# Kernel optimization log

Hardware: AMD Instinct MI355X
Metric: run time of the kernel (lower is better)

Reference implementation:

```python
import jax, jax.numpy as jnp
import numpy as np

B, C_IN, H, W = 4, 256, 256, 256
L = 5000                 # candidate lines per image
N_PTS0, N_PTS1 = 32, 8   # sampled points per line, pooled points
DIM_LOI, DIM_FC = 128, 1024
N_OUT_LINE = 2500


def setup_inputs() -> dict:
    key = jax.random.key(0)
    ks = jax.random.split(key, 8)
    feature = jax.random.normal(ks[0], (B, C_IN, H, W), jnp.float32)
    # line endpoints in [0, 255) pixel coords (row, col)
    lines_in = jax.random.uniform(ks[1], (B, L, 2, 2), jnp.float32) * 255.0
    fc1_w = jax.random.normal(ks[2], (DIM_LOI, C_IN), jnp.float32) * 0.05
    fc1_b = jnp.zeros((DIM_LOI,), jnp.float32)
    w1 = jax.random.normal(ks[3], (DIM_FC, DIM_LOI * N_PTS1), jnp.float32) * 0.02
    b1 = jnp.zeros((DIM_FC,), jnp.float32)
    w2 = jax.random.normal(ks[4], (DIM_FC, DIM_FC), jnp.float32) * 0.02
    b2 = jnp.zeros((DIM_FC,), jnp.float32)
    w3 = jax.random.normal(ks[5], (4, DIM_FC), jnp.float32) * 0.02
    b3 = jnp.zeros((4,), jnp.float32)
    return dict(feature=feature, lines_in=lines_in, fc1_w=fc1_w, fc1_b=fc1_b,
                w1=w1, b1=b1, w2=w2, b2=b2, w3=w3, b3=b3)


def _bilinear_sample(xi, px, py):
    # xi: [C, H, W]; px, py: [P] float coords. Matches torch clamp(0, 255).
    px0 = jnp.clip(jnp.floor(px), 0.0, 255.0)
    py0 = jnp.clip(jnp.floor(py), 0.0, 255.0)
    px1 = jnp.clip(px0 + 1.0, 0.0, 255.0)
    py1 = jnp.clip(py0 + 1.0, 0.0, 255.0)
    px0l, py0l = px0.astype(jnp.int32), py0.astype(jnp.int32)
    px1l, py1l = px1.astype(jnp.int32), py1.astype(jnp.int32)
    xp = (xi[:, px0l, py0l] * (px1 - px) * (py1 - py)
          + xi[:, px1l, py0l] * (px - px0) * (py1 - py)
          + xi[:, px0l, py1l] * (px1 - px) * (py - py0)
          + xi[:, px1l, py1l] * (px - px0) * (py - py0))
    return xp  # [C, P]


def _select(p0, s0, m):
    # p0: [L,2,2], s0: [L,4], m: [L] bool. Threshold-masked, argsort by argmax
    # class (descending), cyclically padded to N_OUT_LINE.
    max_idx = jnp.argmax(s0, axis=1)
    sort_key = jnp.where(m, max_idx, -1)          # unmasked rows sink to the end
    order = jnp.argsort(-sort_key)                # stable, descending by class id
    cnt = m.sum()
    idxs = jnp.arange(N_OUT_LINE) % jnp.maximum(cnt, 1)
    sel = order[idxs]
    li = jnp.where(cnt > 0, p0[sel], jnp.zeros_like(p0[sel]))
    si = jnp.where(cnt > 0, s0[sel], jnp.zeros_like(s0[sel]))
    return li, si


def reference(feature, lines_in, fc1_w, fc1_b, w1, b1, w2, b2, w3, b3):
    # fc1: 1x1 conv -> [B, DIM_LOI, H, W]
    x = jnp.einsum('bchw,oc->bohw', feature, fc1_w) + fc1_b[None, :, None, None]

    # sample N_PTS0 points along each line: p0*lam + p1*(1-lam) - 0.5
    lam = jnp.linspace(0.0, 1.0, N_PTS0, dtype=jnp.float32)[:, None]  # [32,1]
    pts = lines_in[:, :, 0:1, :] * lam + lines_in[:, :, 1:2, :] * (1.0 - lam) - 0.5  # [B,L,32,2]
    px = pts[..., 0].reshape(B, -1)  # [B, L*32]
    py = pts[..., 1].reshape(B, -1)

    xp = jax.vmap(_bilinear_sample)(x, px, py)            # [B, C, L*32]
    xp = xp.reshape(B, DIM_LOI, L, N_PTS0).transpose(0, 2, 1, 3)  # [B, L, C, 32]

    # MaxPool1d(4, 4) over the point axis -> [B, L, C, 8]
    xp = xp.reshape(B, L, DIM_LOI, N_PTS1, N_PTS0 // N_PTS1).max(axis=-1)
    flat = xp.reshape(B, L, DIM_LOI * N_PTS1)

    # fc2 MLP: 1024 -> 1024 -> 1024 -> 4
    h = jax.nn.relu(jnp.einsum('blf,df->bld', flat, w1) + b1)
    h = jax.nn.relu(jnp.einsum('bld,ed->ble', h, w2) + b2)
    logits = jnp.einsum('ble,oe->blo', h, w3) + b3        # [B, L, 4]

    s = jax.nn.softmax(logits, axis=-1)
    mask = ((s[..., 1] > 0.25) | (s[..., 2] > 0.25) | (s[..., 3] > 0.25)) & (s[..., 0] < 0.25)

    lines_out, score_out = jax.vmap(_select)(lines_in, s, mask)
    return lines_out, score_out  # [B, 2500, 2, 2], [B, 2500, 4]
```

## Files before the change

### kernel.cpp

```cpp
#include <hip/hip_runtime.h>
#include <hip/hip_bf16.h>
#include <math.h>

#define BB 4
#define C_IN 256
#define HH 256
#define WW 256
#define LL 5000
#define N_PTS0 32
#define N_PTS1 8
#define DIM_LOI 128
#define DIM_FC 1024
#define N_OUT_LINE 2500
#define MM (BB * LL)
#define PIX (HH * WW)

typedef __attribute__((ext_vector_type(8))) short short8_t;
typedef __attribute__((ext_vector_type(4))) float float4v;

__device__ __forceinline__ short f2bf(float f) {
    union { float f; unsigned u; } c; c.f = f;
    unsigned u = c.u;
    u += 0x7FFFu + ((u >> 16) & 1u);
    return (short)(u >> 16);
}
__device__ __forceinline__ float bf2f(short h) {
    union { unsigned u; float f; } c; c.u = ((unsigned)(unsigned short)h) << 16;
    return c.f;
}

__device__ __forceinline__ void load_lds16(const void* g, void* l) {
    __builtin_amdgcn_global_load_lds(
        (const __attribute__((address_space(1))) void*)g,
        (__attribute__((address_space(3))) void*)l, 16, 0, 0);
}

__device__ __forceinline__ void wave_barrier() {
    asm volatile("" ::: "memory");
    __builtin_amdgcn_s_barrier();
    asm volatile("" ::: "memory");
}

#define MFMA_B16(a, b, c) \
    c = __builtin_amdgcn_mfma_f32_16x16x32_bf16(a, b, c, 0, 0, 0)

__global__ __launch_bounds__(256) void conv_mfma_kernel(
    const float* __restrict__ feat,
    const short* __restrict__ whi,
    const short* __restrict__ wlo,
    const float* __restrict__ bias,
    float* __restrict__ x)
{
    __shared__ short As_hi[128][40];
    __shared__ short As_lo[128][40];
    __shared__ short Ws_hi[128][40];
    __shared__ short Ws_lo[128][40];

    const int t  = threadIdx.x;
    const int m0 = blockIdx.x * 128;
    const int b  = m0 >> 16;
    const int p0 = m0 & (PIX - 1);
    const float* fb = feat + (size_t)b * C_IN * PIX + p0;

    const int w = t >> 6, lane = t & 63;
    const int wmb = (w >> 1) * 64, wnb = (w & 1) * 64;
    const int fr = lane & 15;
    const int koff = (lane >> 4) << 3;

    const int sp = t & 127;
    const int cg = t >> 7;

    float4v acc[4][4];
#pragma unroll
    for (int mi = 0; mi < 4; mi++)
#pragma unroll
        for (int ni = 0; ni < 4; ni++)
            acc[mi][ni] = (float4v){0.f, 0.f, 0.f, 0.f};

    for (int k0 = 0; k0 < C_IN; k0 += 32) {
#pragma unroll
        for (int i = 0; i < 2; i++) {
            int idx = t + (i << 8);
            int row = idx >> 2;
            int kc  = (idx & 3) << 3;
            *(int4*)&Ws_hi[row][kc] = *(const int4*)(whi + row * C_IN + k0 + kc);
            *(int4*)&Ws_lo[row][kc] = *(const int4*)(wlo + row * C_IN + k0 + kc);
        }
#pragma unroll
        for (int j = 0; j < 8; j++) {
            int c = cg * 16 + j * 2;
            float v0 = fb[(size_t)(k0 + c) * PIX + sp];
            float v1 = fb[(size_t)(k0 + c + 1) * PIX + sp];
            short h0 = f2bf(v0), h1 = f2bf(v1);
            short l0 = f2bf(v0 - bf2f(h0)), l1 = f2bf(v1 - bf2f(h1));
            *(unsigned*)&As_hi[sp][c] =
                (unsigned)(unsigned short)h0 | ((unsigned)(unsigned short)h1 << 16);
            *(unsigned*)&As_lo[sp][c] =
                (unsigned)(unsigned short)l0 | ((unsigned)(unsigned short)l1 << 16);
        }
        __syncthreads();

        short8_t ah[4], al[4];
#pragma unroll
        for (int mi = 0; mi < 4; mi++) {
            ah[mi] = *(const short8_t*)&As_hi[wmb + mi * 16 + fr][koff];
            al[mi] = *(const short8_t*)&As_lo[wmb + mi * 16 + fr][koff];
        }
#pragma unroll
        for (int ni = 0; ni < 4; ni++) {
            short8_t bh = *(const short8_t*)&Ws_hi[wnb + ni * 16 + fr][koff];
            short8_t bl = *(const short8_t*)&Ws_lo[wnb + ni * 16 + fr][koff];
#pragma unroll
            for (int mi = 0; mi < 4; mi++) {
                MFMA_B16(ah[mi], bh, acc[mi][ni]);
                MFMA_B16(al[mi], bh, acc[mi][ni]);
                MFMA_B16(ah[mi], bl, acc[mi][ni]);
            }
        }
        __syncthreads();
    }

#pragma unroll
    for (int ni = 0; ni < 4; ni++) {
        int ncol = wnb + ni * 16 + fr;
        float bv = bias[ncol];
#pragma unroll
        for (int mi = 0; mi < 4; mi++) {
            int r0 = m0 + wmb + mi * 16 + ((lane >> 4) << 2);
#pragma unroll
            for (int i2 = 0; i2 < 4; i2++) {
                x[(size_t)(r0 + i2) * 128 + ncol] = acc[mi][ni][i2] + bv;
            }
        }
    }
}

__global__ __launch_bounds__(128) void sample_pool_kernel(
    const float* __restrict__ lines,
    const float* __restrict__ x,
    short* __restrict__ phi,
    short* __restrict__ plo)
{
    const int bl = blockIdx.x;
    const int b  = bl / LL;
    const int c  = threadIdx.x;
    const float* lp = lines + (size_t)bl * 4;
    const float p0r = lp[0], p0c = lp[1], p1r = lp[2], p1c = lp[3];
    const float* xb = x + (size_t)b * PIX * 128;

    short8_t vh, vl;
#pragma unroll
    for (int g = 0; g < 8; g++) {
        float mx = -INFINITY;
#pragma unroll
        for (int j = 0; j < 4; j++) {
            int tt = g * 4 + j;
            float lam = (float)((double)tt / 31.0);
            float px = p0r * lam + p1r * (1.0f - lam) - 0.5f;
            float py = p0c * lam + p1c * (1.0f - lam) - 0.5f;
            float px0 = fminf(fmaxf(floorf(px), 0.0f), 255.0f);
            float py0 = fminf(fmaxf(floorf(py), 0.0f), 255.0f);
            float px1 = fminf(px0 + 1.0f, 255.0f);
            float py1 = fminf(py0 + 1.0f, 255.0f);
            int ix0 = (int)px0, iy0 = (int)py0, ix1 = (int)px1, iy1 = (int)py1;
            float wx1 = px1 - px, wx0 = px - px0;
            float wy1 = py1 - py, wy0 = py - py0;
            float v00 = xb[(size_t)(ix0 * WW + iy0) * 128 + c];
            float v10 = xb[(size_t)(ix1 * WW + iy0) * 128 + c];
            float v01 = xb[(size_t)(ix0 * WW + iy1) * 128 + c];
            float v11 = xb[(size_t)(ix1 * WW + iy1) * 128 + c];
            float v = v00 * (wx1 * wy1) + v10 * (wx0 * wy1)
                    + v01 * (wx1 * wy0) + v11 * (wx0 * wy0);
            mx = fmaxf(mx, v);
        }
        short h = f2bf(mx);
        vh[g] = h;
        vl[g] = f2bf(mx - bf2f(h));
    }
    *(short8_t*)(phi + (size_t)bl * 1024 + c * 8) = vh;
    *(short8_t*)(plo + (size_t)bl * 1024 + c * 8) = vl;
}

__global__ __launch_bounds__(256) void split_kernel(
    const float* __restrict__ w, short* __restrict__ hi, short* __restrict__ lo)
{
    const int i = (blockIdx.x * 256 + threadIdx.x) * 4;
    float4 v = *(const float4*)(w + i);
    float vv[4] = {v.x, v.y, v.z, v.w};
    short4 h, l;
    short hs[4], ls[4];
#pragma unroll
    for (int j = 0; j < 4; j++) {
        hs[j] = f2bf(vv[j]);
        ls[j] = f2bf(vv[j] - bf2f(hs[j]));
    }
    h.x = hs[0]; h.y = hs[1]; h.z = hs[2]; h.w = hs[3];
    l.x = ls[0]; l.y = ls[1]; l.z = ls[2]; l.w = ls[3];
    *(short4*)(hi + i) = h;
    *(short4*)(lo + i) = l;
}

#define NT 32
#define BUF_SHORTS 24576

template <bool SPLIT_OUT>
__global__ __launch_bounds__(512, 2) void gemm_bf16x3_v3(
    const short* __restrict__ Ahi, const short* __restrict__ Alo,
    const short* __restrict__ Bhi, const short* __restrict__ Blo,
    const float* __restrict__ bias,
    float* __restrict__ Cf, short* __restrict__ Chi, short* __restrict__ Clo,
    int M, int Mtiles)
{
    __shared__ short lds[3 * BUF_SHORTS];

    const int t    = threadIdx.x;
    const int bid  = blockIdx.x;
    const int wgid  = (bid & 7) * Mtiles + (bid >> 3);
    const int tileM = wgid >> 3;
    const int tileN = wgid & 7;
    const int m0 = tileM * 256, n0 = tileN * 128;

    const int w = t >> 6, lane = t & 63;
    const int wmb = (w >> 1) * 64;
    const int wnb = (w & 1) * 64;
    const int fr = lane & 15;
    const int ksw = (((lane >> 4) ^ ((lane >> 1) & 3)) << 3);
    const int a_base = (wmb + fr) * 32 + ksw;
    const int b_base = 16384 + (wnb + fr) * 32 + ksw;

    const short* gp[6];
    int lp[6];
    {
        const int csrc = (lane & 3) ^ ((lane >> 3) & 3);
#pragma unroll
        for (int s = 0; s < 6; s++) {
            int e = w * 6 + s;
            int m_ = (e < 16) ? 0 : (e < 32) ? 1 : (e < 40) ? 2 : 3;
            int j  = e - ((m_ == 0) ? 0 : (m_ == 1) ? 16 : (m_ == 2) ? 32 : 40);
            const short* mp = (m_ == 0) ? Ahi : (m_ == 1) ? Alo
                            : (m_ == 2) ? Bhi : Blo;
            int mo = (m_ == 0) ? 0 : (m_ == 1) ? 8192
                   : (m_ == 2) ? 16384 : 20480;
            int row  = j * 16 + (lane >> 2);
            int grow = (m_ < 2) ? min(m0 + row, M - 1) : (n0 + row);
            gp[s] = mp + (size_t)grow * 1024 + csrc * 8;
            lp[s] = mo + j * 512 + lane * 8;
        }
    }

#pragma unroll
    for (int s = 0; s < 6; s++) { load_lds16(gp[s], &lds[lp[s]]); gp[s] += 32; }
#pragma unroll
    for (int s = 0; s < 6; s++) { load_lds16(gp[s], &lds[BUF_SHORTS + lp[s]]); gp[s] += 32; }
    asm volatile("s_waitcnt vmcnt(6)" ::: "memory");
    wave_barrier();

    float4v acc[4][4];
#pragma unroll
    for (int mi = 0; mi < 4; mi++)
#pragma unroll
        for (int ni = 0; ni < 4; ni++)
            acc[mi][ni] = (float4v){0.f, 0.f, 0.f, 0.f};

    int off_cur = 0, off_nxt = BUF_SHORTS, off_pre = 2 * BUF_SHORTS;

    for (int kt = 0; kt < NT; ++kt) {
        const bool pf = (kt + 2 < NT);

        short8_t bh[4], bl[4];
#pragma unroll
        for (int ni = 0; ni < 4; ni++) {
            bh[ni] = *(const short8_t*)&lds[off_cur + b_base + ni * 512];
            bl[ni] = *(const short8_t*)&lds[off_cur + b_base + ni * 512 + 4096];
        }
        short8_t ah = *(const short8_t*)&lds[off_cur + a_base];
        short8_t al = *(const short8_t*)&lds[off_cur + a_base + 8192];
        if (pf) {
            load_lds16(gp[0], &lds[off_pre + lp[0]]); gp[0] += 32;
            load_lds16(gp[1], &lds[off_pre + lp[1]]); gp[1] += 32;
        }
        wave_barrier();
        asm volatile("s_waitcnt lgkmcnt(0)" ::: "memory");
        __builtin_amdgcn_sched_barrier(0);
        __builtin_amdgcn_s_setprio(1);
#pragma unroll
        for (int ni = 0; ni < 4; ni++) {
            MFMA_B16(ah, bh[ni], acc[0][ni]);
            MFMA_B16(al, bh[ni], acc[0][ni]);
            MFMA_B16(ah, bl[ni], acc[0][ni]);
        }
        __builtin_amdgcn_s_setprio(0);
        wave_barrier();

#pragma unroll
        for (int mi = 1; mi < 4; mi++) {
            ah = *(const short8_t*)&lds[off_cur + a_base + mi * 512];
            al = *(const short8_t*)&lds[off_cur + a_base + mi * 512 + 8192];
            if (pf && mi < 3) {
                load_lds16(gp[2 * mi],     &lds[off_pre + lp[2 * mi]]);     gp[2 * mi]     += 32;
                load_lds16(gp[2 * mi + 1], &lds[off_pre + lp[2 * mi + 1]]); gp[2 * mi + 1] += 32;
            }
            wave_barrier();
            asm volatile("s_waitcnt lgkmcnt(0)" ::: "memory");
            __builtin_amdgcn_sched_barrier(0);
            __builtin_amdgcn_s_setprio(1);
#pragma unroll
            for (int ni = 0; ni < 4; ni++) {
                MFMA_B16(ah, bh[ni], acc[mi][ni]);
                MFMA_B16(al, bh[ni], acc[mi][ni]);
                MFMA_B16(ah, bl[ni], acc[mi][ni]);
            }
            __builtin_amdgcn_s_setprio(0);
            if (mi < 3) wave_barrier();
        }

        if (pf) asm volatile("s_waitcnt vmcnt(6)" ::: "memory");
        else    asm volatile("s_waitcnt vmcnt(0)" ::: "memory");
        wave_barrier();
        int tmp = off_cur; off_cur = off_nxt; off_nxt = off_pre; off_pre = tmp;
    }

#pragma unroll
    for (int ni = 0; ni < 4; ni++) {
        int ncol = n0 + wnb + ni * 16 + fr;
        float bv = bias[ncol];
#pragma unroll
        for (int mi = 0; mi < 4; mi++) {
            int r0 = m0 + wmb + mi * 16 + ((lane >> 4) << 2);
#pragma unroll
            for (int i2 = 0; i2 < 4; i2++) {
                int r = r0 + i2;
                if (r < M) {
                    float v = fmaxf(acc[mi][ni][i2] + bv, 0.0f);
                    if (SPLIT_OUT) {
                        short h = f2bf(v);
                        Chi[(size_t)r * 1024 + ncol] = h;
                        Clo[(size_t)r * 1024 + ncol] = f2bf(v - bf2f(h));
                    } else {
                        Cf[(size_t)r * 1024 + ncol] = v;
                    }
                }
            }
        }
    }
}

__global__ __launch_bounds__(256) void fc3_softmax_kernel(
    const float* __restrict__ h2, const float* __restrict__ w3,
    const float* __restrict__ b3, float* __restrict__ s, int* __restrict__ keys)
{
    const int m = blockIdx.x * 4 + (threadIdx.x >> 6);
    const int lane = threadIdx.x & 63;
    const float* hp = h2 + (size_t)m * DIM_FC;
    float a0 = 0.f, a1 = 0.f, a2 = 0.f, a3 = 0.f;
    for (int k = lane; k < DIM_FC; k += 64) {
        float hv = hp[k];
        a0 = fmaf(hv, w3[k], a0);
        a1 = fmaf(hv, w3[DIM_FC + k], a1);
        a2 = fmaf(hv, w3[2 * DIM_FC + k], a2);
        a3 = fmaf(hv, w3[3 * DIM_FC + k], a3);
    }
#pragma unroll
    for (int off = 32; off > 0; off >>= 1) {
        a0 += __shfl_down(a0, off, 64);
        a1 += __shfl_down(a1, off, 64);
        a2 += __shfl_down(a2, off, 64);
        a3 += __shfl_down(a3, off, 64);
    }
    if (lane == 0) {
        float l0 = a0 + b3[0], l1 = a1 + b3[1], l2 = a2 + b3[2], l3 = a3 + b3[3];
        float mxl = fmaxf(fmaxf(l0, l1), fmaxf(l2, l3));
        float e0 = expf(l0 - mxl), e1 = expf(l1 - mxl);
        float e2 = expf(l2 - mxl), e3 = expf(l3 - mxl);
        float inv = 1.0f / (e0 + e1 + e2 + e3);
        float s0 = e0 * inv, s1 = e1 * inv, s2 = e2 * inv, s3 = e3 * inv;
        float* sp = s + (size_t)m * 4;
        sp[0] = s0; sp[1] = s1; sp[2] = s2; sp[3] = s3;
        int best = 0; float bv = s0;
        if (s1 > bv) { best = 1; bv = s1; }
        if (s2 > bv) { best = 2; bv = s2; }
        if (s3 > bv) { best = 3; bv = s3; }
        bool msk = ((s1 > 0.25f) || (s2 > 0.25f) || (s3 > 0.25f)) && (s0 < 0.25f);
        keys[m] = msk ? best : -1;
    }
}

__global__ __launch_bounds__(64) void order_kernel(
    const int* __restrict__ keys, int* __restrict__ ord, int* __restrict__ cnts)
{
    const int b = blockIdx.x;
    const int lane = threadIdx.x;
    const int* kb = keys + b * LL;
    int c0 = 0, c1 = 0, c2 = 0, c3 = 0;
    for (int line = lane; line < LL; line += 64) {
        int k = kb[line];
        c0 += (k == 0); c1 += (k == 1); c2 += (k == 2); c3 += (k == 3);
    }
#pragma unroll
    for (int off = 32; off > 0; off >>= 1) {
        c0 += __shfl_down(c0, off, 64);
        c1 += __shfl_down(c1, off, 64);
        c2 += __shfl_down(c2, off, 64);
        c3 += __shfl_down(c3, off, 64);
    }
    int t0 = __shfl(c0, 0, 64), t1 = __shfl(c1, 0, 64);
    int t2 = __shfl(c2, 0, 64), t3 = __shfl(c3, 0, 64);
    if (lane == 0) cnts[b] = t0 + t1 + t2 + t3;
    int base[4];
    base[3] = 0; base[2] = t3; base[1] = t3 + t2; base[0] = t3 + t2 + t1;
    int run[4] = {0, 0, 0, 0};
    const unsigned long long below = (1ull << lane) - 1ull;
    int* ob = ord + b * LL;
    for (int s0 = 0; s0 < LL; s0 += 64) {
        int line = s0 + lane;
        int k = (line < LL) ? kb[line] : -2;
#pragma unroll
        for (int kk = 0; kk < 4; kk++) {
            unsigned long long mask = __ballot(k == kk);
            if (k == kk) {
                int pos = base[kk] + run[kk] + __popcll(mask & below);
                ob[pos] = line;
            }
            run[kk] += __popcll(mask);
        }
    }
}

__global__ __launch_bounds__(256) void fill_kernel(
    const float* __restrict__ lines, const float* __restrict__ s,
    const int* __restrict__ ord, const int* __restrict__ cnts,
    float* __restrict__ out)
{
    const int i = blockIdx.x * 256 + threadIdx.x;
    if (i >= BB * N_OUT_LINE) return;
    const int b = i / N_OUT_LINE;
    const int j = i % N_OUT_LINE;
    const int cnt = cnts[b];
    float4 lo = {0.f, 0.f, 0.f, 0.f}, sc = {0.f, 0.f, 0.f, 0.f};
    if (cnt > 0) {
        int line = ord[b * LL + (j % cnt)];
        lo = *(const float4*)(lines + ((size_t)b * LL + line) * 4);
        sc = *(const float4*)(s + ((size_t)b * LL + line) * 4);
    }
    *(float4*)(out + (size_t)i * 4) = lo;
    *(float4*)(out + (size_t)(BB * N_OUT_LINE) * 4 + (size_t)i * 4) = sc;
}

extern "C" void kernel_launch(void* const* d_in, const int* in_sizes, int n_in,
                              void* d_out, int out_size, void* d_ws, size_t ws_size,
                              hipStream_t stream) {
    (void)in_sizes; (void)n_in; (void)out_size; (void)ws_size;
    const float* feature = (const float*)d_in[0];
    const float* lines   = (const float*)d_in[1];
    const float* fc1_w   = (const float*)d_in[2];
    const float* fc1_b   = (const float*)d_in[3];
    const float* w1      = (const float*)d_in[4];
    const float* b1      = (const float*)d_in[5];
    const float* w2      = (const float*)d_in[6];
    const float* b2      = (const float*)d_in[7];
    const float* w3      = (const float*)d_in[8];
    const float* b3      = (const float*)d_in[9];
    float* out = (float*)d_out;

    float* x = (float*)d_ws;
    short* pooled_hi = (short*)(x + (size_t)BB * PIX * 128);
    short* pooled_lo = pooled_hi + (size_t)MM * DIM_FC;
    short* h1hi = (short*)x;
    short* h1lo = h1hi + (size_t)MM * DIM_FC;
    float* h2 = (float*)pooled_hi;
    short* w1hi = (short*)((char*)d_ws + 100u * 1024u * 1024u);
    short* w1lo = w1hi + DIM_FC * DIM_FC;
    short* w2hi = w1lo + DIM_FC * DIM_FC;
    short* w2lo = w2hi + DIM_FC * DIM_FC;
    float* s    = (float*)(pooled_lo + (size_t)MM * DIM_FC);
    int* keys   = (int*)(s + MM * 4);
    int* ord    = keys + MM;
    int* cnts   = ord + MM;
    short* fc1hi = (short*)(cnts + 64);
    short* fc1lo = fc1hi + DIM_LOI * C_IN;

    split_kernel<<<(DIM_LOI * C_IN) / 1024, 256, 0, stream>>>(fc1_w, fc1hi, fc1lo);
    conv_mfma_kernel<<<(BB * PIX) / 128, 256, 0, stream>>>(
        feature, fc1hi, fc1lo, fc1_b, x);
    sample_pool_kernel<<<MM, 128, 0, stream>>>(lines, x, pooled_hi, pooled_lo);
    split_kernel<<<DIM_FC * DIM_FC / 1024, 256, 0, stream>>>(w1, w1hi, w1lo);
    split_kernel<<<DIM_FC * DIM_FC / 1024, 256, 0, stream>>>(w2, w2hi, w2lo);

    const int Mtiles = (MM + 255) / 256;
    gemm_bf16x3_v3<true><<<Mtiles * 8, 512, 0, stream>>>(
        pooled_hi, pooled_lo, w1hi, w1lo, b1, nullptr, h1hi, h1lo, MM, Mtiles);
    gemm_bf16x3_v3<false><<<Mtiles * 8, 512, 0, stream>>>(
        h1hi, h1lo, w2hi, w2lo, b2, h2, nullptr, nullptr, MM, Mtiles);

    fc3_softmax_kernel<<<MM / 4, 256, 0, stream>>>(h2, w3, b3, s, keys);
    order_kernel<<<BB, 64, 0, stream>>>(keys, ord, cnts);
    fill_kernel<<<(BB * N_OUT_LINE + 255) / 256, 256, 0, stream>>>(
        lines, s, ord, cnts, out);
}
```

Measured before the change: 934.1 us.

## Enlarge GEMM tiles to 192x256 with double-buffered LDS and XCD-aware mapping

Measured after the change: 890.2 us. -4.7%, faster.

```diff
diff --git a/kernel.cpp b/kernel.cpp
--- a/kernel.cpp
+++ b/kernel.cpp
@@ -201,143 +201,124 @@
 }
 
 #define NT 32
-#define BUF_SHORTS 24576
+#define BUFS 28672
+#define A_LO 6144
+#define B_HI 12288
+#define B_LO 20480
 
 template <bool SPLIT_OUT>
-__global__ __launch_bounds__(512, 2) void gemm_bf16x3_v3(
+__global__ __launch_bounds__(512, 2) void gemm_bf16x3_v4(
     const short* __restrict__ Ahi, const short* __restrict__ Alo,
     const short* __restrict__ Bhi, const short* __restrict__ Blo,
     const float* __restrict__ bias,
     float* __restrict__ Cf, short* __restrict__ Chi, short* __restrict__ Clo,
     int M, int Mtiles)
 {
-    __shared__ short lds[3 * BUF_SHORTS];
-
-    const int t    = threadIdx.x;
-    const int bid  = blockIdx.x;
-    const int wgid  = (bid & 7) * Mtiles + (bid >> 3);
-    const int tileM = wgid >> 3;
-    const int tileN = wgid & 7;
-    const int m0 = tileM * 256, n0 = tileN * 128;
+    __shared__ short lds[2 * BUFS];
+
+    const int t   = threadIdx.x;
+    const int bid = blockIdx.x;
+    const int nwg = Mtiles * 4;
+    const int q = nwg >> 3, r = nwg & 7;
+    const int xcd = bid & 7, seq = bid >> 3;
+    const int wgid = ((xcd < r) ? xcd * (q + 1) : r * (q + 1) + (xcd - r) * q) + seq;
+    const int tileM = wgid >> 2, tileN = wgid & 3;
+    const int m0 = tileM * 192, n0 = tileN * 256;
 
     const int w = t >> 6, lane = t & 63;
-    const int wmb = (w >> 1) * 64;
-    const int wnb = (w & 1) * 64;
+    const int wr = w >> 2;
+    const int wc = w & 3;
     const int fr = lane & 15;
     const int ksw = (((lane >> 4) ^ ((lane >> 1) & 3)) << 3);
-    const int a_base = (wmb + fr) * 32 + ksw;
-    const int b_base = 16384 + (wnb + fr) * 32 + ksw;
-
-    const short* gp[6];
-    int lp[6];
+    const int a_row = wr * 96 + fr;
+    const int b_row = wc * 64 + fr;
+
+    const short* gp[7];
+    int lp[7];
     {
         const int csrc = (lane & 3) ^ ((lane >> 3) & 3);
 #pragma unroll
-        for (int s = 0; s < 6; s++) {
-            int e = w * 6 + s;
-            int m_ = (e < 16) ? 0 : (e < 32) ? 1 : (e < 40) ? 2 : 3;
-            int j  = e - ((m_ == 0) ? 0 : (m_ == 1) ? 16 : (m_ == 2) ? 32 : 40);
-            const short* mp = (m_ == 0) ? Ahi : (m_ == 1) ? Alo
-                            : (m_ == 2) ? Bhi : Blo;
-            int mo = (m_ == 0) ? 0 : (m_ == 1) ? 8192
-                   : (m_ == 2) ? 16384 : 20480;
-            int row  = j * 16 + (lane >> 2);
-            int grow = (m_ < 2) ? min(m0 + row, M - 1) : (n0 + row);
+        for (int s = 0; s < 7; s++) {
+            int e = w * 7 + s;
+            const short* mp; int mo, j, grow;
+            int rl = lane >> 2;
+            if (e < 12)      { mp = Ahi; mo = 0;    j = e;      grow = min(m0 + j * 16 + rl, M - 1); }
+            else if (e < 24) { mp = Alo; mo = A_LO; j = e - 12; grow = min(m0 + j * 16 + rl, M - 1); }
+            else if (e < 40) { mp = Bhi; mo = B_HI; j = e - 24; grow = n0 + j * 16 + rl; }
+            else             { mp = Blo; mo = B_LO; j = e - 40; grow = n0 + j * 16 + rl; }
             gp[s] = mp + (size_t)grow * 1024 + csrc * 8;
             lp[s] = mo + j * 512 + lane * 8;
         }
     }
 
 #pragma unroll
-    for (int s = 0; s < 6; s++) { load_lds16(gp[s], &lds[lp[s]]); gp[s] += 32; }
-#pragma unroll
-    for (int s = 0; s < 6; s++) { load_lds16(gp[s], &lds[BUF_SHORTS + lp[s]]); gp[s] += 32; }
-    asm volatile("s_waitcnt vmcnt(6)" ::: "memory");
+    for (int s = 0; s < 7; s++) { load_lds16(gp[s], &lds[lp[s]]); gp[s] += 32; }
+#pragma unroll
+    for (int s = 0; s < 7; s++) { load_lds16(gp[s], &lds[BUFS + lp[s]]); gp[s] += 32; }
+    asm volatile("s_waitcnt vmcnt(7)" ::: "memory");
     wave_barrier();
 
-    float4v acc[4][4];
-#pragma unroll
-    for (int mi = 0; mi < 4; mi++)
-#pragma unroll
-        for (int ni = 0; ni < 4; ni++)
-            acc[mi][ni] = (float4v){0.f, 0.f, 0.f, 0.f};
-
-    int off_cur = 0, off_nxt = BUF_SHORTS, off_pre = 2 * BUF_SHORTS;
+    float4v acc[6][4];
+#pragma unroll
+    for (int mf = 0; mf < 6; mf++)
+#pragma unroll
+        for (int nf = 0; nf < 4; nf++)
+            acc[mf][nf] = (float4v){0.f, 0.f, 0.f, 0.f};
 
     for (int kt = 0; kt < NT; ++kt) {
-        const bool pf = (kt + 2 < NT);
+        const int off = (kt & 1) * BUFS;
 
         short8_t bh[4], bl[4];
 #pragma unroll
-        for (int ni = 0; ni < 4; ni++) {
-            bh[ni] = *(const short8_t*)&lds[off_cur + b_base + ni * 512];
-            bl[ni] = *(const short8_t*)&lds[off_cur + b_base + ni * 512 + 4096];
-        }
-        short8_t ah = *(const short8_t*)&lds[off_cur + a_base];
-        short8_t al = *(const short8_t*)&lds[off_cur + a_base + 8192];
-        if (pf) {
-            load_lds16(gp[0], &lds[off_pre + lp[0]]); gp[0] += 32;
-            load_lds16(gp[1], &lds[off_pre + lp[1]]); gp[1] += 32;
-        }
-        wave_barrier();
-        asm volatile("s_waitcnt lgkmcnt(0)" ::: "memory");
-        __builtin_amdgcn_sched_barrier(0);
-        __builtin_amdgcn_s_setprio(1);
-#pragma unroll
-        for (int ni = 0; ni < 4; ni++) {
-            MFMA_B16(ah, bh[ni], acc[0][ni]);
-            MFMA_B16(al, bh[ni], acc[0][ni]);
-            MFMA_B16(ah, bl[ni], acc[0][ni]);
-        }
-        __builtin_amdgcn_s_setprio(0);
-        wave_barrier();
-
-#pragma unroll
-        for (int mi = 1; mi < 4; mi++) {
-            ah = *(const short8_t*)&lds[off_cur + a_base + mi * 512];
-            al = *(const short8_t*)&lds[off_cur + a_base + mi * 512 + 8192];
-            if (pf && mi < 3) {
-                load_lds16(gp[2 * mi],     &lds[off_pre + lp[2 * mi]]);     gp[2 * mi]     += 32;
-                load_lds16(gp[2 * mi + 1], &lds[off_pre + lp[2 * mi + 1]]); gp[2 * mi + 1] += 32;
-            }
+        for (int nf = 0; nf < 4; nf++) {
+            bh[nf] = *(const short8_t*)&lds[off + B_HI + (b_row + nf * 16) * 32 + ksw];
+            bl[nf] = *(const short8_t*)&lds[off + B_LO + (b_row + nf * 16) * 32 + ksw];
+        }
+#pragma unroll
+        for (int mf = 0; mf < 6; mf++) {
+            short8_t ah = *(const short8_t*)&lds[off + (a_row + mf * 16) * 32 + ksw];
+            short8_t al = *(const short8_t*)&lds[off + A_LO + (a_row + mf * 16) * 32 + ksw];
+#pragma unroll
+            for (int nf = 0; nf < 4; nf++) {
+                MFMA_B16(ah, bh[nf], acc[mf][nf]);
+                MFMA_B16(al, bh[nf], acc[mf][nf]);
+                MFMA_B16(ah, bl[nf], acc[mf][nf]);
+            }
+        }
+
+        if (kt < NT - 1) {
             wave_barrier();
-            asm volatile("s_waitcnt lgkmcnt(0)" ::: "memory");
-            __builtin_amdgcn_sched_barrier(0);
-            __builtin_amdgcn_s_setprio(1);
-#pragma unroll
-            for (int ni = 0; ni < 4; ni++) {
-                MFMA_B16(ah, bh[ni], acc[mi][ni]);
-                MFMA_B16(al, bh[ni], acc[mi][ni]);
-                MFMA_B16(ah, bl[ni], acc[mi][ni]);
-            }
-            __builtin_amdgcn_s_setprio(0);
-            if (mi < 3) wave_barrier();
-        }
-
-        if (pf) asm volatile("s_waitcnt vmcnt(6)" ::: "memory");
-        else    asm volatile("s_waitcnt vmcnt(0)" ::: "memory");
-        wave_barrier();
-        int tmp = off_cur; off_cur = off_nxt; off_nxt = off_pre; off_pre = tmp;
-    }
-
-#pragma unroll
-    for (int ni = 0; ni < 4; ni++) {
-        int ncol = n0 + wnb + ni * 16 + fr;
+            if (kt + 2 < NT) {
+#pragma unroll
+                for (int s = 0; s < 7; s++) {
+                    load_lds16(gp[s], &lds[off + lp[s]]); gp[s] += 32;
+                }
+                asm volatile("s_waitcnt vmcnt(7)" ::: "memory");
+            } else {
+                asm volatile("s_waitcnt vmcnt(0)" ::: "memory");
+            }
+            wave_barrier();
+        }
+    }
+
+#pragma unroll
+    for (int nf = 0; nf < 4; nf++) {
+        int ncol = n0 + wc * 64 + nf * 16 + fr;
         float bv = bias[ncol];
 #pragma unroll
-        for (int mi = 0; mi < 4; mi++) {
-            int r0 = m0 + wmb + mi * 16 + ((lane >> 4) << 2);
+        for (int mf = 0; mf < 6; mf++) {
+            int r0 = m0 + wr * 96 + mf * 16 + ((lane >> 4) << 2);
 #pragma unroll
             for (int i2 = 0; i2 < 4; i2++) {
-                int r = r0 + i2;
-                if (r < M) {
-                    float v = fmaxf(acc[mi][ni][i2] + bv, 0.0f);
+                int rr = r0 + i2;
+                if (rr < M) {
+                    float v = fmaxf(acc[mf][nf][i2] + bv, 0.0f);
                     if (SPLIT_OUT) {
                         short h = f2bf(v);
-                        Chi[(size_t)r * 1024 + ncol] = h;
-                        Clo[(size_t)r * 1024 + ncol] = f2bf(v - bf2f(h));
+                        Chi[(size_t)rr * 1024 + ncol] = h;
+                        Clo[(size_t)rr * 1024 + ncol] = f2bf(v - bf2f(h));
                     } else {
-                        Cf[(size_t)r * 1024 + ncol] = v;
+                        Cf[(size_t)rr * 1024 + ncol] = v;
                     }
                 }
             }
@@ -486,10 +467,10 @@
     split_kernel<<<DIM_FC * DIM_FC / 1024, 256, 0, stream>>>(w1, w1hi, w1lo);
     split_kernel<<<DIM_FC * DIM_FC / 1024, 256, 0, stream>>>(w2, w2hi, w2lo);
 
-    const int Mtiles = (MM + 255) / 256;
-    gemm_bf16x3_v3<true><<<Mtiles * 8, 512, 0, stream>>>(
+    const int Mtiles = (MM + 191) / 192;
+    gemm_bf16x3_v4<true><<<Mtiles * 4, 512, 0, stream>>>(
         pooled_hi, pooled_lo, w1hi, w1lo, b1, nullptr, h1hi, h1lo, MM, Mtiles);
-    gemm_bf16x3_v3<false><<<Mtiles * 8, 512, 0, stream>>>(
+    gemm_bf16x3_v4<false><<<Mtiles * 4, 512, 0, stream>>>(
         h1hi, h1lo, w2hi, w2lo, b2, h2, nullptr, nullptr, MM, Mtiles);
 
     fc3_softmax_kernel<<<MM / 4, 256, 0, stream>>>(h2, w3, b3, s, keys);
```
